# Optimization experiments

Hardware: AMD Instinct MI355X
Metric: run time of the kernel (lower is better)

## Reference

```python
import jax, jax.numpy as jnp
import numpy as np

BETA = 0.25
K = 1024   # num_codebook_vectors
D = 256    # latent_dim


def setup_inputs() -> dict:
    key = jax.random.key(0)
    k1, k2 = jax.random.split(key)
    z = jax.random.normal(k1, (16, D, 64, 64), dtype=jnp.float32)
    # embedding initialized uniform(-1/K, 1/K) as in the torch module
    emb = jax.random.uniform(k2, (K, D), dtype=jnp.float32, minval=-1.0 / K, maxval=1.0 / K)
    return {"z": z, "emb": emb}


def reference(z, emb):
    sg = jax.lax.stop_gradient
    # NCHW -> NHWC
    z_nhwc = jnp.transpose(z, (0, 2, 3, 1))            # [B,H,W,D]
    zf = z_nhwc.reshape(-1, D)                          # [N,D]
    # squared euclidean distances: ||z||^2 + ||e||^2 - 2 z e^T
    d = (jnp.sum(zf * zf, axis=1, keepdims=True)
         + jnp.sum(emb * emb, axis=1)
         - 2.0 * jnp.matmul(zf, emb.T))                 # [N,K]
    min_encoding_indices = jnp.argmin(d, axis=1)        # [N] int
    z_q = emb[min_encoding_indices].reshape(z_nhwc.shape)  # [B,H,W,D]
    # loss exactly as in source (first term is zero in value, faithful)
    loss = (jnp.mean((sg(z_nhwc) - z_nhwc) ** 2)
            + BETA * jnp.mean((z_q - sg(z_nhwc)) ** 2))
    # straight-through estimator
    z_q_st = z_nhwc + sg(z_q - z_nhwc)
    out = jnp.transpose(z_q_st, (0, 3, 1, 2))           # NHWC -> NCHW
    return out, min_encoding_indices, loss
```

## Files before the change

### kernel.cpp

```cpp
#include <hip/hip_runtime.h>

#define DD 256
#define KK 1024
#define HW 4096
#define NROWSZ 65536
#define OUT_Z 16777216
#define OUT_IDX OUT_Z
#define OUT_LOSS (OUT_Z + NROWSZ)

#define MARGIN 4.5e-4f

#define WS_ESQ   0
#define WS_EH    4096
#define WS_HLIST 528384
#define WS_HCNT  790528
#define WS_LSUM  790536
#define WS_EMBT  791552
#define WS_EHP   1840128

typedef _Float16 f16x8 __attribute__((ext_vector_type(8)));
typedef float f32x4 __attribute__((ext_vector_type(4)));
union U16x8 { uint4 u; f16x8 h; };
typedef unsigned long long u64;

static __device__ __forceinline__ u64 umin64(u64 a, u64 b) { return a < b ? a : b; }
static __device__ __forceinline__ unsigned pk16(float a, float b) {
    _Float16 ha = (_Float16)a, hb = (_Float16)b;
    return (unsigned)__builtin_bit_cast(unsigned short, ha)
         | ((unsigned)__builtin_bit_cast(unsigned short, hb) << 16);
}

__global__ void vq_prep(const float* __restrict__ emb, float* __restrict__ esq,
                        uint2* __restrict__ eh2, int* __restrict__ hcnt,
                        double* __restrict__ lsum, float* __restrict__ embT,
                        int use_embT, uint4* __restrict__ ehP, int use_ehp)
{
    const int bid = blockIdx.x;
    const int t = threadIdx.x;
    if (bid == 0 && t == 0) { *hcnt = 0; *lsum = 0.0; }

    if (bid < 4) {
        int k = bid * 256 + t;
        const float* e = emb + (size_t)k * DD;
        float blk[2];
#pragma unroll
        for (int b2 = 0; b2 < 2; ++b2) {
            const float* p = e + b2 * 128;
            float r[8];
#pragma unroll
            for (int j = 0; j < 8; ++j) r[j] = __fmul_rn(p[j], p[j]);
            for (int i = 8; i < 128; i += 8) {
#pragma unroll
                for (int j = 0; j < 8; ++j)
                    r[j] = __fadd_rn(r[j], __fmul_rn(p[i + j], p[i + j]));
            }
            blk[b2] = __fadd_rn(__fadd_rn(__fadd_rn(r[0], r[1]), __fadd_rn(r[2], r[3])),
                                __fadd_rn(__fadd_rn(r[4], r[5]), __fadd_rn(r[6], r[7])));
        }
        esq[k] = __fadd_rn(blk[0], blk[1]);
    } else if (bid < 20) {
        int tid = (bid - 4) * 256 + t;
        const float4* e4 = (const float4*)emb;
#pragma unroll
        for (int i = 0; i < 16; ++i) {
            int idx = i * 4096 + tid;
            float4 v = e4[idx];
            eh2[idx] = make_uint2(pk16(v.x, v.y), pk16(v.z, v.w));
        }
    } else if (bid < 36) {
        if (!use_embT) return;
        int u = bid - 20;
        int k = u * 64 + (t >> 2);
        int c = t & 3;
        const float4* e4 = (const float4*)(emb + (size_t)k * DD);
#pragma unroll
        for (int i = 0; i < 16; ++i) {
            float4 v = e4[c * 16 + i];
            int d = c * 64 + i * 4;
            embT[(size_t)(d + 0) * KK + k] = v.x;
            embT[(size_t)(d + 1) * KK + k] = v.y;
            embT[(size_t)(d + 2) * KK + k] = v.z;
            embT[(size_t)(d + 3) * KK + k] = v.w;
        }
    } else {
        if (!use_ehp) return;
#pragma unroll
        for (int it = 0; it < 8; ++it) {
            int L = ((bid - 36) * 8 + it) * 256 + t;
            int lane = L & 63, ds = (L >> 6) & 7, t16 = L >> 9;
            int col = lane & 15, quad = lane >> 4;
            int code = t16 * 16 + col;
            int d0 = ds * 32 + quad * 8;
            const float* e = emb + (size_t)code * DD + d0;
            float4 a = *(const float4*)e;
            float4 c4 = *(const float4*)(e + 4);
            ehP[L] = make_uint4(pk16(a.x, a.y), pk16(a.z, a.w),
                                pk16(c4.x, c4.y), pk16(c4.z, c4.w));
        }
    }
}

__launch_bounds__(256, 2)
__global__ void vq_score(const float* __restrict__ z, const _Float16* __restrict__ eh,
                         const uint4* __restrict__ ehP, const float* __restrict__ esq,
                         float* __restrict__ out, int* __restrict__ hlist,
                         int* __restrict__ hcnt, int use_ehp)
{
    __shared__ __align__(16) char zh[64 * 512];
    __shared__ float esq_s[1024];
    __shared__ uint2 cand[128];

    const int t = threadIdx.x;
    const int lane = t & 63;
    const int w = t >> 6;
    const int col = lane & 15;
    const int quad = lane >> 4;

    const int n0 = blockIdx.x * 128;
    const int b = n0 >> 12;
    const int hw0 = n0 & (HW - 1);

    esq_s[t] = esq[t];
    esq_s[256 + t] = esq[256 + t];
    esq_s[512 + t] = esq[512 + t];
    esq_s[768 + t] = esq[768 + t];

    U16x8 af[2][8];
    {
        const int rl = t & 63, dg = t >> 6;
#pragma unroll
        for (int c = 0; c < 2; ++c) {
            const float* src = z + (size_t)b * DD * HW + hw0 + c * 64 + rl;
#pragma unroll
            for (int i = 0; i < 2; ++i) {
                const int d0 = dg * 64 + i * 32;
#pragma unroll
                for (int j = 0; j < 4; ++j) {
                    const int dd = d0 + j * 8;
                    float v0 = src[(size_t)(dd + 0) * HW];
                    float v1 = src[(size_t)(dd + 1) * HW];
                    float v2 = src[(size_t)(dd + 2) * HW];
                    float v3 = src[(size_t)(dd + 3) * HW];
                    float v4 = src[(size_t)(dd + 4) * HW];
                    float v5 = src[(size_t)(dd + 5) * HW];
                    float v6 = src[(size_t)(dd + 6) * HW];
                    float v7 = src[(size_t)(dd + 7) * HW];
                    uint4 pk = make_uint4(pk16(v0, v1), pk16(v2, v3),
                                          pk16(v4, v5), pk16(v6, v7));
                    *(uint4*)(zh + (size_t)rl * 512 + ((dd * 2) ^ ((rl & 7) << 4))) = pk;
                }
            }
            __syncthreads();
            if ((w >> 1) == c) {
#pragma unroll
                for (int nt = 0; nt < 2; ++nt) {
                    const int lr = (w & 1) * 32 + nt * 16 + col;
                    const int sw = (lr & 7) << 4;
#pragma unroll
                    for (int ds = 0; ds < 8; ++ds)
                        af[nt][ds].u = *(const uint4*)(zh + (size_t)lr * 512
                                                       + ((ds * 64 + quad * 16) ^ sw));
                }
            }
            __syncthreads();
        }
    }

    unsigned t1[8], t2[8];
#pragma unroll
    for (int i = 0; i < 8; ++i) { t1[i] = 0xFFFFFFFFu; t2[i] = 0xFFFFFFFFu; }

    auto proc = [&](U16x8 (&bf)[8], int t16) {
        const int code = t16 * 16 + col;
        const float eq1 = 1.0f + esq_s[code];
        f32x4 acc0 = (f32x4)0.0f, acc1 = (f32x4)0.0f;
#pragma unroll
        for (int ds = 0; ds < 8; ++ds) {
            acc0 = __builtin_amdgcn_mfma_f32_16x16x32_f16(af[0][ds].h, bf[ds].h, acc0, 0, 0, 0);
            acc1 = __builtin_amdgcn_mfma_f32_16x16x32_f16(af[1][ds].h, bf[ds].h, acc1, 0, 0, 0);
        }
#pragma unroll
        for (int r = 0; r < 4; ++r) {
            float s0 = fmaf(-2.0f, acc0[r], eq1);
            unsigned k0 = (__float_as_uint(s0) & 0xFFFFFC00u) | (unsigned)code;
            t2[r] = min(t2[r], max(t1[r], k0));
            t1[r] = min(t1[r], k0);
            float s1 = fmaf(-2.0f, acc1[r], eq1);
            unsigned k1 = (__float_as_uint(s1) & 0xFFFFFC00u) | (unsigned)code;
            t2[4 + r] = min(t2[4 + r], max(t1[4 + r], k1));
            t1[4 + r] = min(t1[4 + r], k1);
        }
    };

    if (use_ehp) {
        const uint4* bq = ehP + lane;
        U16x8 bfA[8], bfB[8];
#pragma unroll
        for (int ds = 0; ds < 8; ++ds) bfA[ds].u = bq[ds * 64];
#pragma unroll 1
        for (int t16 = 0; t16 < 64; t16 += 2) {
            const uint4* p1 = bq + (size_t)(t16 + 1) * 512;
#pragma unroll
            for (int ds = 0; ds < 8; ++ds) bfB[ds].u = p1[ds * 64];
            proc(bfA, t16);
            const uint4* p2 = bq + (size_t)((t16 + 2) & 63) * 512;
#pragma unroll
            for (int ds = 0; ds < 8; ++ds) bfA[ds].u = p2[ds * 64];
            proc(bfB, t16 + 1);
            if ((t16 & 6) == 6) __builtin_amdgcn_s_barrier();
        }
    } else {
        const uint4* ehq = (const uint4*)eh;
#pragma unroll 1
        for (int t16 = 0; t16 < 64; ++t16) {
            const uint4* bp = ehq + (size_t)(t16 * 16 + col) * 32 + quad;
            U16x8 bf[8];
#pragma unroll
            for (int ds = 0; ds < 8; ++ds) bf[ds].u = bp[ds * 4];
            proc(bf, t16);
        }
    }

#pragma unroll
    for (int mi = 0; mi < 8; ++mi) {
        unsigned a = t1[mi], bb = t2[mi];
#pragma unroll
        for (int off = 1; off < 16; off <<= 1) {
            unsigned o1 = __shfl_xor(a, off, 16);
            unsigned o2 = __shfl_xor(bb, off, 16);
            unsigned mx = max(a, o1);
            a = min(a, o1);
            bb = min(min(bb, o2), mx);
        }
        if (col == 0)
            cand[w * 32 + (mi >> 2) * 16 + quad * 4 + (mi & 3)] = make_uint2(a, bb);
    }
    __syncthreads();

    if (t < 128) {
        uint2 c = cand[t];
        float s1 = __uint_as_float(c.x & 0xFFFFFC00u);
        float s2 = __uint_as_float(c.y & 0xFFFFFC00u);
        int k1 = (int)(c.x & 1023u);
        if (__fsub_rn(s2, s1) > MARGIN) {
            out[OUT_IDX + n0 + t] = (float)k1;
        } else {
            int pos = atomicAdd(hcnt, 1);
            hlist[pos] = n0 + t;
        }
    }
}

template<int USET>
static __device__ __forceinline__ void dot_codes(const float4* __restrict__ embT4,
                                                 const float4* __restrict__ emb4,
                                                 const float4* __restrict__ zb4,
                                                 int t, float (&acc_)[8][4])
{
#pragma unroll 2
    for (int dc = 0; dc < 64; ++dc) {
        float4 e0, e1, e2, e3;
        if (USET) {
            e0 = embT4[(size_t)(dc * 4 + 0) * 256 + t];
            e1 = embT4[(size_t)(dc * 4 + 1) * 256 + t];
            e2 = embT4[(size_t)(dc * 4 + 2) * 256 + t];
            e3 = embT4[(size_t)(dc * 4 + 3) * 256 + t];
        } else {
            float4 a0 = emb4[(size_t)(4 * t + 0) * 64 + dc];
            float4 a1 = emb4[(size_t)(4 * t + 1) * 64 + dc];
            float4 a2 = emb4[(size_t)(4 * t + 2) * 64 + dc];
            float4 a3 = emb4[(size_t)(4 * t + 3) * 64 + dc];
            e0 = make_float4(a0.x, a1.x, a2.x, a3.x);
            e1 = make_float4(a0.y, a1.y, a2.y, a3.y);
            e2 = make_float4(a0.z, a1.z, a2.z, a3.z);
            e3 = make_float4(a0.w, a1.w, a2.w, a3.w);
        }
#pragma unroll
        for (int j = 0; j < 8; ++j) {
            float4 zv = zb4[j * 64 + dc];
            acc_[j][0] = fmaf(zv.x, e0.x, acc_[j][0]);
            acc_[j][1] = fmaf(zv.x, e0.y, acc_[j][1]);
            acc_[j][2] = fmaf(zv.x, e0.z, acc_[j][2]);
            acc_[j][3] = fmaf(zv.x, e0.w, acc_[j][3]);
            acc_[j][0] = fmaf(zv.y, e1.x, acc_[j][0]);
            acc_[j][1] = fmaf(zv.y, e1.y, acc_[j][1]);
            acc_[j][2] = fmaf(zv.y, e1.z, acc_[j][2]);
            acc_[j][3] = fmaf(zv.y, e1.w, acc_[j][3]);
            acc_[j][0] = fmaf(zv.z, e2.x, acc_[j][0]);
            acc_[j][1] = fmaf(zv.z, e2.y, acc_[j][1]);
            acc_[j][2] = fmaf(zv.z, e2.z, acc_[j][2]);
            acc_[j][3] = fmaf(zv.z, e2.w, acc_[j][3]);
            acc_[j][0] = fmaf(zv.w, e3.x, acc_[j][0]);
            acc_[j][1] = fmaf(zv.w, e3.y, acc_[j][1]);
            acc_[j][2] = fmaf(zv.w, e3.z, acc_[j][2]);
            acc_[j][3] = fmaf(zv.w, e3.w, acc_[j][3]);
        }
    }
}

__launch_bounds__(256)
__global__ void vq_hard(const float* __restrict__ z, const float* __restrict__ emb,
                        const float* __restrict__ embT, const float* __restrict__ esq,
                        const int* __restrict__ hlist, const int* __restrict__ hcnt,
                        float* __restrict__ out, int use_embT)
{
    __shared__ __align__(16) float zbuf[8 * 256];
    __shared__ float chains[8][16];
    __shared__ float zq_s[8];
    __shared__ int rows_s[8];
    __shared__ u64 red[4][8];

    const int t = threadIdx.x;
    const int lane = t & 63;
    const int w = t >> 6;
    const int count = *hcnt;

    const float4* embT4 = (const float4*)embT;
    const float4* emb4 = (const float4*)emb;
    const float4* zb4 = (const float4*)zbuf;
    const float4 eqv4 = ((const float4*)esq)[t];
    const float eqa[4] = {eqv4.x, eqv4.y, eqv4.z, eqv4.w};

    for (int g = blockIdx.x; g * 8 < count; g += gridDim.x) {
        __syncthreads();
        if (t < 8) {
            int p = g * 8 + t;
            rows_s[t] = (p < count) ? hlist[p] : -1;
        }
        __syncthreads();

        {
            const int j = t >> 5, dpos = t & 31;
            const int r = rows_s[j];
            float4 v0 = make_float4(0.f, 0.f, 0.f, 0.f), v1 = v0;
            if (r >= 0) {
                const float* zp = z + (size_t)(r >> 12) * (DD * HW) + (r & (HW - 1));
                const int d0 = dpos * 8;
                v0.x = zp[(size_t)(d0 + 0) * HW];
                v0.y = zp[(size_t)(d0 + 1) * HW];
                v0.z = zp[(size_t)(d0 + 2) * HW];
                v0.w = zp[(size_t)(d0 + 3) * HW];
                v1.x = zp[(size_t)(d0 + 4) * HW];
                v1.y = zp[(size_t)(d0 + 5) * HW];
                v1.z = zp[(size_t)(d0 + 6) * HW];
                v1.w = zp[(size_t)(d0 + 7) * HW];
            }
            *(float4*)&zbuf[j * 256 + dpos * 8] = v0;
            *(float4*)&zbuf[j * 256 + dpos * 8 + 4] = v1;
        }
        __syncthreads();

        if (t < 128) {
            int j = t >> 4, c = t & 15, b2 = c >> 3, jj = c & 7;
            const float* p = &zbuf[j * 256];
            int base = b2 * 128 + jj;
            float v = p[base];
            float acc = __fmul_rn(v, v);
            for (int i = 1; i < 16; ++i) {
                float u = p[base + i * 8];
                acc = __fadd_rn(acc, __fmul_rn(u, u));
            }
            chains[j][c] = acc;
        }
        __syncthreads();
        if (t < 8) {
            const float* c = chains[t];
            float b0 = __fadd_rn(__fadd_rn(__fadd_rn(c[0], c[1]), __fadd_rn(c[2], c[3])),
                                 __fadd_rn(__fadd_rn(c[4], c[5]), __fadd_rn(c[6], c[7])));
            float b1 = __fadd_rn(__fadd_rn(__fadd_rn(c[8], c[9]), __fadd_rn(c[10], c[11])),
                                 __fadd_rn(__fadd_rn(c[12], c[13]), __fadd_rn(c[14], c[15])));
            zq_s[t] = __fadd_rn(b0, b1);
        }
        __syncthreads();

        float acc_[8][4];
#pragma unroll
        for (int j = 0; j < 8; ++j)
#pragma unroll
            for (int kk = 0; kk < 4; ++kk) acc_[j][kk] = 0.0f;

        if (use_embT) dot_codes<1>(embT4, emb4, zb4, t, acc_);
        else          dot_codes<0>(embT4, emb4, zb4, t, acc_);

#pragma unroll
        for (int j = 0; j < 8; ++j) {
            u64 m = ~0ull;
#pragma unroll
            for (int kk = 0; kk < 4; ++kk) {
                float s = __fsub_rn(__fadd_rn(zq_s[j], eqa[kk]),
                                    __fmul_rn(2.0f, acc_[j][kk]));
                u64 p = ((u64)__float_as_uint(s) << 32) | (unsigned)(4 * t + kk);
                m = umin64(m, p);
            }
#pragma unroll
            for (int off = 1; off < 64; off <<= 1)
                m = umin64(m, __shfl_xor(m, off, 64));
            if (lane == 0) red[w][j] = m;
        }
        __syncthreads();
        if (t < 8) {
            u64 m = umin64(umin64(red[0][t], red[1][t]), umin64(red[2][t], red[3][t]));
            int r = rows_s[t];
            if (r >= 0) out[OUT_IDX + r] = (float)(int)(m & 0xffffffffu);
        }
    }
}

__launch_bounds__(256)
__global__ void vq_out(const float* __restrict__ z, const float* __restrict__ emb,
                       const float* __restrict__ embT, float* out,
                       double* __restrict__ lsum, int use_embT)
{
    __shared__ float et[4 * 1024];
    __shared__ float wsum[4];

    const int t = threadIdx.x;
    const int lane = t & 63;
    const int w = t >> 6;
    const int bb = blockIdx.x >> 6;
    const int dg = blockIdx.x & 63;

    if (use_embT) {
#pragma unroll
        for (int c = 0; c < 4; ++c)
            *(float4*)&et[c * 1024 + t * 4] =
                *(const float4*)&embT[(size_t)(dg * 4 + c) * KK + t * 4];
    } else {
        for (int i = 0; i < 16; ++i) {
            int kk = i * 256 + t;
            et[kk] = emb[(size_t)(kk & 1023) * DD + dg * 4 + (kk >> 10)];
        }
    }
    __syncthreads();

    float lacc = 0.f;
    const size_t zb = (size_t)bb * DD * HW;
    const float* idxf = out + OUT_IDX + (size_t)bb * HW;
#pragma unroll
    for (int ch = 0; ch < 4; ++ch) {
        const int hw = ch * 1024 + t * 4;
        float4 fi = *(const float4*)&idxf[hw];
        int k0 = (int)fi.x, k1 = (int)fi.y, k2 = (int)fi.z, k3 = (int)fi.w;
#pragma unroll
        for (int dl = 0; dl < 4; ++dl) {
            size_t off = zb + (size_t)(dg * 4 + dl) * HW + hw;
            float4 zv = *(const float4*)&z[off];
            float4 e;
            e.x = et[dl * 1024 + k0];
            e.y = et[dl * 1024 + k1];
            e.z = et[dl * 1024 + k2];
            e.w = et[dl * 1024 + k3];
            *(float4*)&out[off] = e;
            float df;
            df = e.x - zv.x; lacc = fmaf(df, df, lacc);
            df = e.y - zv.y; lacc = fmaf(df, df, lacc);
            df = e.z - zv.z; lacc = fmaf(df, df, lacc);
            df = e.w - zv.w; lacc = fmaf(df, df, lacc);
        }
    }
#pragma unroll
    for (int off = 32; off > 0; off >>= 1) lacc += __shfl_down(lacc, off, 64);
    if (lane == 0) wsum[w] = lacc;
    __syncthreads();
    if (t == 0) {
        double tot = (double)wsum[0] + (double)wsum[1] + (double)wsum[2] + (double)wsum[3];
        atomicAdd(lsum, tot);
    }
}

__global__ void vq_final(const double* __restrict__ lsum, float* __restrict__ out)
{
    out[OUT_LOSS] = (float)(0.25 * (lsum[0] / (double)OUT_Z));
}

extern "C" void kernel_launch(void* const* d_in, const int* in_sizes, int n_in,
                              void* d_out, int out_size, void* d_ws, size_t ws_size,
                              hipStream_t stream)
{
    const float* z = (const float*)d_in[0];
    const float* emb = (const float*)d_in[1];
    float* out = (float*)d_out;
    char* w = (char*)d_ws;

    float* esq = (float*)(w + WS_ESQ);
    _Float16* eh = (_Float16*)(w + WS_EH);
    uint2* eh2 = (uint2*)(w + WS_EH);
    int* hlist = (int*)(w + WS_HLIST);
    int* hcnt = (int*)(w + WS_HCNT);
    double* lsum = (double*)(w + WS_LSUM);
    float* embT = (float*)(w + WS_EMBT);
    uint4* ehP = (uint4*)(w + WS_EHP);

    int use_embT = (ws_size >= (size_t)WS_EMBT + (size_t)DD * KK * sizeof(float)) ? 1 : 0;
    int use_ehp = (ws_size >= (size_t)WS_EHP + (size_t)KK * DD * sizeof(_Float16)) ? 1 : 0;

    vq_prep<<<dim3(52), dim3(256), 0, stream>>>(emb, esq, eh2, hcnt, lsum, embT, use_embT,
                                                ehP, use_ehp);
    vq_score<<<dim3(512), dim3(256), 0, stream>>>(z, eh, ehP, esq, out, hlist, hcnt,
                                                  use_ehp);
    vq_hard<<<dim3(1024), dim3(256), 0, stream>>>(z, emb, embT, esq, hlist, hcnt, out,
                                                  use_embT);
    vq_out<<<dim3(1024), dim3(256), 0, stream>>>(z, emb, embT, out, lsum, use_embT);
    vq_final<<<dim3(1), dim3(1), 0, stream>>>(lsum, out);
}
```

Before: 252.2 us.

## Stage codebook tiles into LDS with async global_load_lds double buffering

The packed fp16 codebook fragments are now copied into shared memory with direct global-to-LDS async loads, double-buffered across pairs of 16-code tiles. Before, each wave loaded them into registers straight from global memory. The zh buffer is reused as the staging area, and occupancy is raised to 3 blocks per SM. The goal is to share codebook loads across the four waves and free registers. The cost is a block-wide barrier on every iteration, plus LDS read traffic that competes with the MFMA work.

Result: slower. 258.5 us (+2.5%).

```diff
diff --git a/kernel.cpp b/kernel.cpp
--- a/kernel.cpp
+++ b/kernel.cpp
@@ -28,6 +28,11 @@
     _Float16 ha = (_Float16)a, hb = (_Float16)b;
     return (unsigned)__builtin_bit_cast(unsigned short, ha)
          | ((unsigned)__builtin_bit_cast(unsigned short, hb) << 16);
+}
+static __device__ __forceinline__ void gl_lds16(const void* g, void* l) {
+    __builtin_amdgcn_global_load_lds(
+        (const __attribute__((address_space(1))) unsigned int*)g,
+        (__attribute__((address_space(3))) unsigned int*)l, 16, 0, 0);
 }
 
 __global__ void vq_prep(const float* __restrict__ emb, float* __restrict__ esq,
@@ -100,15 +105,16 @@
     }
 }
 
-__launch_bounds__(256, 2)
+__launch_bounds__(256, 3)
 __global__ void vq_score(const float* __restrict__ z, const _Float16* __restrict__ eh,
                          const uint4* __restrict__ ehP, const float* __restrict__ esq,
                          float* __restrict__ out, int* __restrict__ hlist,
                          int* __restrict__ hcnt, int use_ehp)
 {
-    __shared__ __align__(16) char zh[64 * 512];
-    __shared__ float esq_s[1024];
-    __shared__ uint2 cand[128];
+    __shared__ __align__(16) char smem[37888];
+    char* zh = smem;
+    float* esq_s = (float*)(smem + 32768);
+    uint2* cand = (uint2*)(smem + 36864);
 
     const int t = threadIdx.x;
     const int lane = t & 63;
@@ -170,7 +176,11 @@
 #pragma unroll
     for (int i = 0; i < 8; ++i) { t1[i] = 0xFFFFFFFFu; t2[i] = 0xFFFFFFFFu; }
 
-    auto proc = [&](U16x8 (&bf)[8], int t16) {
+    auto proc = [&](const char* bbuf, int t16) {
+        U16x8 bf[8];
+#pragma unroll
+        for (int ds = 0; ds < 8; ++ds)
+            bf[ds].u = *(const uint4*)(bbuf + ds * 1024 + lane * 16);
         const int code = t16 * 16 + col;
         const float eq1 = 1.0f + esq_s[code];
         f32x4 acc0 = (f32x4)0.0f, acc1 = (f32x4)0.0f;
@@ -193,21 +203,24 @@
     };
 
     if (use_ehp) {
-        const uint4* bq = ehP + lane;
-        U16x8 bfA[8], bfB[8];
-#pragma unroll
-        for (int ds = 0; ds < 8; ++ds) bfA[ds].u = bq[ds * 64];
+        const char* ehB = (const char*)ehP;
+        auto stage = [&](int tp, int sel) {
+            const char* src = ehB + (size_t)tp * 16384 + (w * 4) * 1024 + lane * 16;
+            char* dst = smem + sel * 16384 + (w * 4) * 1024;
+#pragma unroll
+            for (int i = 0; i < 4; ++i)
+                gl_lds16(src + i * 1024, dst + i * 1024);
+        };
+        stage(0, 0);
+        __syncthreads();
 #pragma unroll 1
-        for (int t16 = 0; t16 < 64; t16 += 2) {
-            const uint4* p1 = bq + (size_t)(t16 + 1) * 512;
-#pragma unroll
-            for (int ds = 0; ds < 8; ++ds) bfB[ds].u = p1[ds * 64];
-            proc(bfA, t16);
-            const uint4* p2 = bq + (size_t)((t16 + 2) & 63) * 512;
-#pragma unroll
-            for (int ds = 0; ds < 8; ++ds) bfA[ds].u = p2[ds * 64];
-            proc(bfB, t16 + 1);
-            if ((t16 & 6) == 6) __builtin_amdgcn_s_barrier();
+        for (int tp = 0; tp < 32; ++tp) {
+            const int cur = tp & 1;
+            if (tp + 1 < 32) stage(tp + 1, cur ^ 1);
+            const char* bb = smem + cur * 16384;
+            proc(bb, tp * 2);
+            proc(bb + 8192, tp * 2 + 1);
+            __syncthreads();
         }
     } else {
         const uint4* ehq = (const uint4*)eh;
@@ -217,7 +230,25 @@
             U16x8 bf[8];
 #pragma unroll
             for (int ds = 0; ds < 8; ++ds) bf[ds].u = bp[ds * 4];
-            proc(bf, t16);
+            const int code = t16 * 16 + col;
+            const float eq1 = 1.0f + esq_s[code];
+            f32x4 acc0 = (f32x4)0.0f, acc1 = (f32x4)0.0f;
+#pragma unroll
+            for (int ds = 0; ds < 8; ++ds) {
+                acc0 = __builtin_amdgcn_mfma_f32_16x16x32_f16(af[0][ds].h, bf[ds].h, acc0, 0, 0, 0);
+                acc1 = __builtin_amdgcn_mfma_f32_16x16x32_f16(af[1][ds].h, bf[ds].h, acc1, 0, 0, 0);
+            }
+#pragma unroll
+            for (int r = 0; r < 4; ++r) {
+                float s0 = fmaf(-2.0f, acc0[r], eq1);
+                unsigned k0 = (__float_as_uint(s0) & 0xFFFFFC00u) | (unsigned)code;
+                t2[r] = min(t2[r], max(t1[r], k0));
+                t1[r] = min(t1[r], k0);
+                float s1 = fmaf(-2.0f, acc1[r], eq1);
+                unsigned k1 = (__float_as_uint(s1) & 0xFFFFFC00u) | (unsigned)code;
+                t2[4 + r] = min(t2[4 + r], max(t1[4 + r], k1));
+                t1[4 + r] = min(t1[4 + r], k1);
+            }
         }
     }
 
```
